# Performance work log

Measured on AMD Instinct MI355X. Metric: run time of the kernel, lower is better.

Reference implementation:

```python
import jax, jax.numpy as jnp
import numpy as np

N_NODES = 100000
N_EDGES = 1600000
D = 128
BN_EPS = 1e-5


def setup_inputs() -> dict:
    key = jax.random.key(0)
    ks = jax.random.split(key, 6)
    x = jax.random.normal(ks[0], (N_NODES, D), dtype=jnp.float32)
    edge_index = jax.random.randint(ks[1], (2, N_EDGES), 0, N_NODES, dtype=jnp.int64)
    s = 1.0 / np.sqrt(D)
    W1 = jax.random.uniform(ks[2], (D, D), jnp.float32, -s, s)
    W2 = jax.random.uniform(ks[3], (D, D), jnp.float32, -s, s)
    b1 = jnp.zeros((D,), jnp.float32)
    b2 = jnp.zeros((D,), jnp.float32)
    gamma = jnp.ones((D,), jnp.float32)
    beta = jnp.zeros((D,), jnp.float32)
    return {"x": x, "edge_index": edge_index, "W1": W1, "b1": b1,
            "W2": W2, "b2": b2, "gamma": gamma, "beta": beta}


def reference(x, edge_index, W1, b1, W2, b2, gamma, beta):
    src = edge_index[0]
    dst = edge_index[1]
    # GIN aggregation: (1+eps)*x + sum_{j in N(i)} x_j, eps = 0
    agg = jax.ops.segment_sum(x[src], dst, num_segments=x.shape[0])  # [N, D]
    h = agg + x
    # 2-layer MLP
    h = jax.nn.relu(h @ W1 + b1) @ W2 + b2
    # BatchNorm1d (training-mode batch stats, biased variance)
    mean = jnp.mean(h, axis=0)
    var = jnp.mean(jnp.square(h - mean), axis=0)
    h = (h - mean) * jax.lax.rsqrt(var + BN_EPS) * gamma + beta
    # residual; dropout p=0 -> identity
    return h + x
```

## Files before the change

### kernel.cpp

```cpp
#include <hip/hip_runtime.h>
#include <math.h>

#define NNODES 100000
#define NEDGES 1600000
#define DD 128
#define BN_EPS 1e-5f

#define NBUCK 98
#define BUCKW 1024
#define PBLK 512
#define PCHUNK 3125
#define NTILES 1563
#define FMM_GRID 512

typedef __attribute__((ext_vector_type(8))) short bf16x8;
typedef __attribute__((ext_vector_type(4))) float f32x4;
typedef __attribute__((ext_vector_type(2))) unsigned u32x2;
typedef __attribute__((ext_vector_type(4))) unsigned u32x4;

__device__ __forceinline__ unsigned short f2bf(float f) {
  unsigned u = __builtin_bit_cast(unsigned, f);
  u = (u + 0x7fffu + ((u >> 16) & 1u)) >> 16;
  return (unsigned short)u;
}
__device__ __forceinline__ float bfLO(unsigned u) {
  return __builtin_bit_cast(float, u << 16);
}
__device__ __forceinline__ float bfHI(unsigned u) {
  return __builtin_bit_cast(float, u & 0xffff0000u);
}


__global__ __launch_bounds__(256) void k_prep(const float* __restrict__ x,
                                              const float* __restrict__ W1,
                                              const float* __restrict__ W2,
                                              unsigned short* __restrict__ xb,
                                              unsigned short* __restrict__ wt1,
                                              unsigned short* __restrict__ wt2,
                                              float* __restrict__ bnAcc,
                                              const int* __restrict__ e32,
                                              int* __restrict__ cnt) {
  __shared__ int sc[NBUCK];
  int bid = blockIdx.x, tid = threadIdx.x;
  if (bid < 2) {
    const float* W = bid ? W2 : W1;
    unsigned short* wt = bid ? wt2 : wt1;
    if (tid < 128) {
      int n = tid;
      for (int k = 0; k < 128; ++k)
        wt[n * 128 + (k ^ ((n & 7) << 3))] = f2bf(W[k * 128 + n]);
    } else {
      bnAcc[(bid ? 0 : 128) + (tid - 128)] = 0.f;
    }
  } else if (bid < 6252) {
    long j = (long)(bid - 2) * 2048 + tid * 8;
    f32x4 a = __builtin_nontemporal_load((const f32x4*)(x + j));
    f32x4 b = __builtin_nontemporal_load((const f32x4*)(x + j + 4));
    u32x4 o;
    o.x = (unsigned)f2bf(a.x) | ((unsigned)f2bf(a.y) << 16);
    o.y = (unsigned)f2bf(a.z) | ((unsigned)f2bf(a.w) << 16);
    o.z = (unsigned)f2bf(b.x) | ((unsigned)f2bf(b.y) << 16);
    o.w = (unsigned)f2bf(b.z) | ((unsigned)f2bf(b.w) << 16);
    *(u32x4*)(xb + j) = o;
  } else {
    int blk = bid - 6252;
    int z = (tid < 64) ? (e32[2 * tid + 1] == 0) : 1;
    int is64 = __syncthreads_and(z);
    for (int i = tid; i < NBUCK; i += 256) sc[i] = 0;
    __syncthreads();
    const int* dstp = is64 ? (e32 + 2 * (long)NEDGES) : (e32 + NEDGES);
    long e0 = (long)blk * PCHUNK;
    for (int i = tid; i < PCHUNK; i += 256) {
      long e = e0 + i;
      int d = is64 ? dstp[2 * e] : dstp[e];
      atomicAdd(&sc[d >> 10], 1);
    }
    __syncthreads();
    for (int i = tid; i < NBUCK; i += 256) cnt[i * PBLK + blk] = sc[i];
  }
}

__global__ __launch_bounds__(256) void k_lscan(const int* __restrict__ cnt,
                                               int* __restrict__ off,
                                               int* __restrict__ bucketTot) {
  __shared__ int s[256];
  int b = blockIdx.x, tid = threadIdx.x;
  int v0 = cnt[b * PBLK + 2 * tid], v1 = cnt[b * PBLK + 2 * tid + 1];
  s[tid] = v0 + v1;
  __syncthreads();
  for (int o = 1; o < 256; o <<= 1) {
    int v = (tid >= o) ? s[tid - o] : 0;
    __syncthreads();
    s[tid] += v;
    __syncthreads();
  }
  int excl = s[tid] - v0 - v1;
  off[b * PBLK + 2 * tid] = excl;
  off[b * PBLK + 2 * tid + 1] = excl + v0;
  if (tid == 255) bucketTot[b] = s[255];
}

__global__ __launch_bounds__(256) void k_ppart(const int* __restrict__ e32,
                                               const int* __restrict__ off,
                                               const int* __restrict__ bucketTot,
                                               unsigned* __restrict__ stage) {
  __shared__ int cur[NBUCK];
  __shared__ int sbase[128];
  int tid = threadIdx.x, blk = blockIdx.x;
  int z = (tid < 64) ? (e32[2 * tid + 1] == 0) : 1;
  int is64 = __syncthreads_and(z);
  if (tid < 128) sbase[tid] = (tid < NBUCK) ? bucketTot[tid] : 0;
  __syncthreads();
  for (int o = 1; o < 128; o <<= 1) {
    int v = (tid >= o && tid < 128) ? sbase[tid - o] : 0;
    __syncthreads();
    if (tid < 128) sbase[tid] += v;
    __syncthreads();
  }
  if (tid < NBUCK)
    cur[tid] = off[tid * PBLK + blk] + ((tid == 0) ? 0 : sbase[tid - 1]);
  __syncthreads();
  const int* dstp = is64 ? (e32 + 2 * (long)NEDGES) : (e32 + NEDGES);
  long e0 = (long)blk * PCHUNK;
  for (int i = tid; i < PCHUNK; i += 256) {
    long e = e0 + i;
    int d = is64 ? dstp[2 * e] : dstp[e];
    int sv = is64 ? e32[2 * e] : e32[e];
    int pos = atomicAdd(&cur[d >> 10], 1);
    stage[pos] = ((unsigned)sv << 10) | (unsigned)(d & (BUCKW - 1));
  }
}

__global__ __launch_bounds__(256) void k_bucket(const unsigned* __restrict__ stage,
                                                const int* __restrict__ bucketTot,
                                                int* __restrict__ rowPtr,
                                                int* __restrict__ edgeSrc) {
  __shared__ int sdeg[BUCKW];
  __shared__ int srow[BUCKW];
  __shared__ int ss[256];
  __shared__ int sbase[128];
  int b = blockIdx.x, tid = threadIdx.x;
  if (tid < 128) sbase[tid] = (tid < NBUCK) ? bucketTot[tid] : 0;
  for (int i = tid; i < BUCKW; i += 256) sdeg[i] = 0;
  __syncthreads();
  for (int o = 1; o < 128; o <<= 1) {
    int v = (tid >= o && tid < 128) ? sbase[tid - o] : 0;
    __syncthreads();
    if (tid < 128) sbase[tid] += v;
    __syncthreads();
  }
  int base = (b == 0) ? 0 : sbase[b - 1];
  int tot = bucketTot[b];
  if (b == 0 && tid == 0) rowPtr[NNODES] = NEDGES;
  const unsigned* st = stage + base;
  for (int i = tid; i < tot; i += 256) atomicAdd(&sdeg[st[i] & (BUCKW - 1)], 1);
  __syncthreads();
  int j = tid * 4;
  int d0 = sdeg[j], d1 = sdeg[j + 1], d2 = sdeg[j + 2], d3 = sdeg[j + 3];
  int tsum = d0 + d1 + d2 + d3;
  ss[tid] = tsum;
  __syncthreads();
  for (int o = 1; o < 256; o <<= 1) {
    int v = (tid >= o) ? ss[tid - o] : 0;
    __syncthreads();
    ss[tid] += v;
    __syncthreads();
  }
  int excl = ss[tid] - tsum;
  srow[j] = excl;
  srow[j + 1] = excl + d0;
  srow[j + 2] = excl + d0 + d1;
  srow[j + 3] = excl + d0 + d1 + d2;
  __syncthreads();
  for (int i = tid; i < BUCKW; i += 256) {
    int dst = b * BUCKW + i;
    if (dst < NNODES) rowPtr[dst] = base + srow[i];
    sdeg[i] = srow[i];
  }
  __syncthreads();
  for (int i = tid; i < tot; i += 256) {
    unsigned p = st[i];
    int pos = atomicAdd(&sdeg[p & (BUCKW - 1)], 1);
    edgeSrc[base + pos] = (int)(p >> 10);
  }
}

__global__ __launch_bounds__(256) void k_gather(const u32x4* __restrict__ xb4,
                                                const int* __restrict__ rowPtr,
                                                const int* __restrict__ edgeSrc,
                                                u32x4* __restrict__ h0b4) {
  int node = (blockIdx.x * 256 + threadIdx.x) >> 6;
  int lane = threadIdx.x & 63;
  if (node >= NNODES) return;
  int li = lane & 15, q = lane >> 4;
  int beg = rowPtr[node], end = rowPtr[node + 1];
  float a0 = 0.f, a1 = 0.f, a2 = 0.f, a3 = 0.f;
  float a4 = 0.f, a5 = 0.f, a6 = 0.f, a7 = 0.f;
#define ACC8(v)                                              \
  a0 += bfLO((v).x); a1 += bfHI((v).x);                      \
  a2 += bfLO((v).y); a3 += bfHI((v).y);                      \
  a4 += bfLO((v).z); a5 += bfHI((v).z);                      \
  a6 += bfLO((v).w); a7 += bfHI((v).w);
  if (q == 0) {
    u32x4 u = xb4[(long)node * 16 + li];
    ACC8(u)
  }
  int e = beg;
  for (; e + 16 <= end; e += 16) {
    int s0 = edgeSrc[e + q];
    int s1 = edgeSrc[e + 4 + q];
    int s2 = edgeSrc[e + 8 + q];
    int s3 = edgeSrc[e + 12 + q];
    u32x4 v0 = xb4[(long)s0 * 16 + li];
    u32x4 v1 = xb4[(long)s1 * 16 + li];
    u32x4 v2 = xb4[(long)s2 * 16 + li];
    u32x4 v3 = xb4[(long)s3 * 16 + li];
    ACC8(v0) ACC8(v1) ACC8(v2) ACC8(v3)
  }
  if (e + 8 <= end) {
    int s0 = edgeSrc[e + q];
    int s1 = edgeSrc[e + 4 + q];
    u32x4 v0 = xb4[(long)s0 * 16 + li];
    u32x4 v1 = xb4[(long)s1 * 16 + li];
    ACC8(v0) ACC8(v1)
    e += 8;
  }
  for (; e < end; e += 4) {
    if (q < end - e) {
      int s = edgeSrc[e + q];
      u32x4 v = xb4[(long)s * 16 + li];
      ACC8(v)
    }
  }
#undef ACC8
  a0 += __shfl_xor(a0, 16, 64); a0 += __shfl_xor(a0, 32, 64);
  a1 += __shfl_xor(a1, 16, 64); a1 += __shfl_xor(a1, 32, 64);
  a2 += __shfl_xor(a2, 16, 64); a2 += __shfl_xor(a2, 32, 64);
  a3 += __shfl_xor(a3, 16, 64); a3 += __shfl_xor(a3, 32, 64);
  a4 += __shfl_xor(a4, 16, 64); a4 += __shfl_xor(a4, 32, 64);
  a5 += __shfl_xor(a5, 16, 64); a5 += __shfl_xor(a5, 32, 64);
  a6 += __shfl_xor(a6, 16, 64); a6 += __shfl_xor(a6, 32, 64);
  a7 += __shfl_xor(a7, 16, 64); a7 += __shfl_xor(a7, 32, 64);
  if (q == 0) {
    u32x4 o;
    o.x = (unsigned)f2bf(a0) | ((unsigned)f2bf(a1) << 16);
    o.y = (unsigned)f2bf(a2) | ((unsigned)f2bf(a3) << 16);
    o.z = (unsigned)f2bf(a4) | ((unsigned)f2bf(a5) << 16);
    o.w = (unsigned)f2bf(a6) | ((unsigned)f2bf(a7) << 16);
    h0b4[(long)node * 16 + li] = o;
  }
}

__global__ __launch_bounds__(256) void k_fmm(const unsigned short* Ab,
                                             const unsigned short* __restrict__ Wt1,
                                             const unsigned short* __restrict__ Wt2,
                                             const float* __restrict__ b1,
                                             const float* __restrict__ b2,
                                             unsigned short* Cb,
                                             float* __restrict__ bnSum,
                                             float* __restrict__ bnSq) {
  __shared__ __align__(16) char smem[81920];
  unsigned short* sW1 = (unsigned short*)smem;
  unsigned short* sW2 = (unsigned short*)(smem + 32768);
  unsigned short* sH  = (unsigned short*)(smem + 65536);
  float* sbn = (float*)(smem + 65536);
  int tid = threadIdx.x;
#pragma unroll
  for (int i = 0; i < 8; ++i) {
    ((u32x4*)sW1)[tid + 256 * i] = ((const u32x4*)Wt1)[tid + 256 * i];
    ((u32x4*)sW2)[tid + 256 * i] = ((const u32x4*)Wt2)[tid + 256 * i];
  }
  int w = tid >> 6, lane = tid & 63, l4 = lane >> 4, l15 = lane & 15;
  float bb1[8], bb2[8], ls[8], lq[8];
#pragma unroll
  for (int ni = 0; ni < 8; ++ni) {
    bb1[ni] = b1[ni * 16 + l15];
    bb2[ni] = b2[ni * 16 + l15];
    ls[ni] = 0.f; lq[ni] = 0.f;
  }

  int tile = blockIdx.x;
  bf16x8 af[4];
  {
    int r = tile * 64 + w * 16 + l15;
    if (r > NNODES - 1) r = NNODES - 1;
#pragma unroll
    for (int ks = 0; ks < 4; ++ks)
      af[ks] = __builtin_nontemporal_load(
          (const bf16x8*)(Ab + (long)r * 128 + ks * 32 + l4 * 8));
  }
  __syncthreads();

  while (tile < NTILES) {
    int next = tile + FMM_GRID;
    f32x4 acc[8];
#pragma unroll
    for (int ni = 0; ni < 8; ++ni) acc[ni] = (f32x4){0.f, 0.f, 0.f, 0.f};
#pragma unroll
    for (int ks = 0; ks < 4; ++ks)
#pragma unroll
      for (int ni = 0; ni < 8; ++ni) {
        int n = ni * 16 + l15, k = ks * 32 + l4 * 8;
        bf16x8 bf = *(const bf16x8*)(sW1 + n * 128 + (k ^ ((n & 7) << 3)));
        acc[ni] = __builtin_amdgcn_mfma_f32_16x16x32_bf16(af[ks], bf, acc[ni], 0, 0, 0);
      }
    __syncthreads();
#pragma unroll
    for (int ni = 0; ni < 8; ++ni) {
      int col = ni * 16 + l15;
#pragma unroll
      for (int rr = 0; rr < 4; ++rr) {
        int row = w * 16 + l4 * 4 + rr;
        float v = fmaxf(acc[ni][rr] + bb1[ni], 0.f);
        sH[row * 128 + (col ^ ((row & 7) << 3))] = f2bf(v);
      }
    }
    __syncthreads();
    bf16x8 afn[4] = {af[0], af[1], af[2], af[3]};
    if (next < NTILES) {
      int r = next * 64 + w * 16 + l15;
      if (r > NNODES - 1) r = NNODES - 1;
#pragma unroll
      for (int ks = 0; ks < 4; ++ks)
        afn[ks] = __builtin_nontemporal_load(
            (const bf16x8*)(Ab + (long)r * 128 + ks * 32 + l4 * 8));
    }
    bf16x8 a2[4];
    {
      int row = w * 16 + l15;
#pragma unroll
      for (int ks = 0; ks < 4; ++ks) {
        int k = ks * 32 + l4 * 8;
        a2[ks] = *(const bf16x8*)(sH + row * 128 + (k ^ ((row & 7) << 3)));
      }
    }
#pragma unroll
    for (int ni = 0; ni < 8; ++ni) acc[ni] = (f32x4){0.f, 0.f, 0.f, 0.f};
#pragma unroll
    for (int ks = 0; ks < 4; ++ks)
#pragma unroll
      for (int ni = 0; ni < 8; ++ni) {
        int n = ni * 16 + l15, k = ks * 32 + l4 * 8;
        bf16x8 bf = *(const bf16x8*)(sW2 + n * 128 + (k ^ ((n & 7) << 3)));
        acc[ni] = __builtin_amdgcn_mfma_f32_16x16x32_bf16(a2[ks], bf, acc[ni], 0, 0, 0);
      }
#pragma unroll
    for (int ni = 0; ni < 8; ++ni) {
      int n = ni * 16 + l15;
#pragma unroll
      for (int rr = 0; rr < 4; ++rr) {
        int row = tile * 64 + w * 16 + l4 * 4 + rr;
        if (row < NNODES) {
          float v = acc[ni][rr] + bb2[ni];
          __builtin_nontemporal_store(f2bf(v), Cb + (long)row * 128 + n);
          ls[ni] += v; lq[ni] += v * v;
        }
      }
    }
#pragma unroll
    for (int ks = 0; ks < 4; ++ks) af[ks] = afn[ks];
    tile = next;
  }

#pragma unroll
  for (int j = 0; j < 8; ++j) {
    ls[j] += __shfl_xor(ls[j], 16, 64); ls[j] += __shfl_xor(ls[j], 32, 64);
    lq[j] += __shfl_xor(lq[j], 16, 64); lq[j] += __shfl_xor(lq[j], 32, 64);
  }
  __syncthreads();
  if (l4 == 0) {
#pragma unroll
    for (int j = 0; j < 8; ++j) {
      sbn[w * 256 + j * 16 + l15] = ls[j];
      sbn[w * 256 + 128 + j * 16 + l15] = lq[j];
    }
  }
  __syncthreads();
  {
    float t = sbn[tid] + sbn[256 + tid] + sbn[512 + tid] + sbn[768 + tid];
    if (tid < 128) atomicAdd(&bnSum[tid], t);
    else atomicAdd(&bnSq[tid - 128], t);
  }
}

__global__ __launch_bounds__(256) void k_epi(const u32x4* __restrict__ h2b4,
                                             const u32x4* __restrict__ xb4,
                                             const float* __restrict__ bnSum,
                                             const float* __restrict__ bnSq,
                                             const float* __restrict__ gamma,
                                             const float* __restrict__ beta,
                                             f32x4* __restrict__ out4) {
  __shared__ float ssc[128], ssh[128];
  int tid = threadIdx.x;
  if (tid < 128) {
    float m = bnSum[tid] * (1.0f / NNODES);
    float var = bnSq[tid] * (1.0f / NNODES) - m * m;
    float sc = gamma[tid] * rsqrtf(var + BN_EPS);
    ssc[tid] = sc;
    ssh[tid] = beta[tid] - m * sc;
  }
  __syncthreads();
  long j = (long)blockIdx.x * 256 + tid;
  int c = (int)((j * 8) & 127);
  u32x4 h = __builtin_nontemporal_load(h2b4 + j);
  u32x4 xr = __builtin_nontemporal_load(xb4 + j);
  f32x4 sa = *(f32x4*)(ssc + c), sb = *(f32x4*)(ssc + c + 4);
  f32x4 fa = *(f32x4*)(ssh + c), fb = *(f32x4*)(ssh + c + 4);
  f32x4 oa, ob;
  oa.x = fmaf(bfLO(h.x), sa.x, fa.x) + bfLO(xr.x);
  oa.y = fmaf(bfHI(h.x), sa.y, fa.y) + bfHI(xr.x);
  oa.z = fmaf(bfLO(h.y), sa.z, fa.z) + bfLO(xr.y);
  oa.w = fmaf(bfHI(h.y), sa.w, fa.w) + bfHI(xr.y);
  ob.x = fmaf(bfLO(h.z), sb.x, fb.x) + bfLO(xr.z);
  ob.y = fmaf(bfHI(h.z), sb.y, fb.y) + bfHI(xr.z);
  ob.z = fmaf(bfLO(h.w), sb.z, fb.z) + bfLO(xr.w);
  ob.w = fmaf(bfHI(h.w), sb.w, fb.w) + bfHI(xr.w);
  __builtin_nontemporal_store(oa, out4 + 2 * j);
  __builtin_nontemporal_store(ob, out4 + 2 * j + 1);
}

extern "C" void kernel_launch(void* const* d_in, const int* in_sizes, int n_in,
                              void* d_out, int out_size, void* d_ws, size_t ws_size,
                              hipStream_t stream) {
  const float* x     = (const float*)d_in[0];
  const int*   e32   = (const int*)d_in[1];
  const float* W1    = (const float*)d_in[2];
  const float* b1    = (const float*)d_in[3];
  const float* W2    = (const float*)d_in[4];
  const float* b2    = (const float*)d_in[5];
  const float* gamma = (const float*)d_in[6];
  const float* beta  = (const float*)d_in[7];
  float* out = (float*)d_out;

  char* ws = (char*)d_ws;
  const size_t BFB = (size_t)NNODES * DD * 2;
  unsigned short* xb  = (unsigned short*)ws;
  unsigned short* h0b = (unsigned short*)(ws + BFB);
  unsigned short* h2b = h0b;

  int* rowPtr     = (int*)(ws + 3 * BFB);
  int* edgeSrc    = rowPtr + NNODES + 4;
  unsigned* stage = (unsigned*)(edgeSrc + NEDGES);
  int* cnt        = (int*)(stage + NEDGES);
  int* off        = cnt + NBUCK * PBLK;
  int* bucketTot  = off + NBUCK * PBLK;

  unsigned short* wt1 = (unsigned short*)(bucketTot + 256);
  unsigned short* wt2 = wt1 + 16384;
  float* bnSum = (float*)(wt2 + 16384);
  float* bnSq  = bnSum + 128;

  k_prep<<<6764, 256, 0, stream>>>(x, W1, W2, xb, wt1, wt2, bnSum, e32, cnt);
  k_lscan<<<NBUCK, 256, 0, stream>>>(cnt, off, bucketTot);
  k_ppart<<<PBLK, 256, 0, stream>>>(e32, off, bucketTot, stage);
  k_bucket<<<NBUCK, 256, 0, stream>>>(stage, bucketTot, rowPtr, edgeSrc);
  k_gather<<<25000, 256, 0, stream>>>((const u32x4*)xb, rowPtr, edgeSrc,
                                      (u32x4*)h0b);
  k_fmm<<<FMM_GRID, 256, 0, stream>>>(h0b, wt1, wt2, b1, b2, h2b, bnSum, bnSq);
  k_epi<<<6250, 256, 0, stream>>>((const u32x4*)h2b, (const u32x4*)xb, bnSum,
                                  bnSq, gamma, beta, (f32x4*)out);
}
```

Before: 196.0 us.

## Fuse BatchNorm epilogue into MLP kernel via grid-wide barrier

Merges the separate epilogue kernel into the fused-MLP kernel. After the BN statistics atomics, a software grid barrier (an atomic counter reset in the prep kernel) waits for all 512 blocks, then each block normalizes its own tiles and writes the output. The h2 bf16 stores become regular stores so they are likely to stay in cache for the epilogue re-read. This removes one kernel launch and may improve cache reuse of h2. In exchange it relies on all 512 blocks being co-resident, since the spin barrier deadlocks otherwise.

```diff
diff --git a/kernel.cpp b/kernel.cpp
--- a/kernel.cpp
+++ b/kernel.cpp
@@ -39,7 +39,8 @@
                                               unsigned short* __restrict__ wt2,
                                               float* __restrict__ bnAcc,
                                               const int* __restrict__ e32,
-                                              int* __restrict__ cnt) {
+                                              int* __restrict__ cnt,
+                                              int* __restrict__ bar) {
   __shared__ int sc[NBUCK];
   int bid = blockIdx.x, tid = threadIdx.x;
   if (bid < 2) {
@@ -51,6 +52,7 @@
         wt[n * 128 + (k ^ ((n & 7) << 3))] = f2bf(W[k * 128 + n]);
     } else {
       bnAcc[(bid ? 0 : 128) + (tid - 128)] = 0.f;
+      if (bid == 0 && tid == 128) *bar = 0;
     }
   } else if (bid < 6252) {
     long j = (long)(bid - 2) * 2048 + tid * 8;
@@ -252,13 +254,18 @@
 }
 
 __global__ __launch_bounds__(256) void k_fmm(const unsigned short* Ab,
+                                             const unsigned short* __restrict__ xb,
                                              const unsigned short* __restrict__ Wt1,
                                              const unsigned short* __restrict__ Wt2,
                                              const float* __restrict__ b1,
                                              const float* __restrict__ b2,
+                                             const float* __restrict__ gamma,
+                                             const float* __restrict__ beta,
                                              unsigned short* Cb,
                                              float* __restrict__ bnSum,
-                                             float* __restrict__ bnSq) {
+                                             float* __restrict__ bnSq,
+                                             int* __restrict__ bar,
+                                             float* __restrict__ outp) {
   __shared__ __align__(16) char smem[81920];
   unsigned short* sW1 = (unsigned short*)smem;
   unsigned short* sW2 = (unsigned short*)(smem + 32768);
@@ -352,7 +359,7 @@
         int row = tile * 64 + w * 16 + l4 * 4 + rr;
         if (row < NNODES) {
           float v = acc[ni][rr] + bb2[ni];
-          __builtin_nontemporal_store(f2bf(v), Cb + (long)row * 128 + n);
+          Cb[(long)row * 128 + n] = f2bf(v);
           ls[ni] += v; lq[ni] += v * v;
         }
       }
@@ -381,42 +388,58 @@
     if (tid < 128) atomicAdd(&bnSum[tid], t);
     else atomicAdd(&bnSq[tid - 128], t);
   }
-}
-
-__global__ __launch_bounds__(256) void k_epi(const u32x4* __restrict__ h2b4,
-                                             const u32x4* __restrict__ xb4,
-                                             const float* __restrict__ bnSum,
-                                             const float* __restrict__ bnSq,
-                                             const float* __restrict__ gamma,
-                                             const float* __restrict__ beta,
-                                             f32x4* __restrict__ out4) {
-  __shared__ float ssc[128], ssh[128];
-  int tid = threadIdx.x;
+
+  __threadfence();
+  __syncthreads();
+  if (tid == 0) {
+    __hip_atomic_fetch_add(bar, 1, __ATOMIC_ACQ_REL, __HIP_MEMORY_SCOPE_AGENT);
+    while (__hip_atomic_load(bar, __ATOMIC_ACQUIRE, __HIP_MEMORY_SCOPE_AGENT) <
+           FMM_GRID)
+      __builtin_amdgcn_s_sleep(8);
+  }
+  __syncthreads();
+
+  float* ssc = sbn;
+  float* ssh = sbn + 128;
   if (tid < 128) {
-    float m = bnSum[tid] * (1.0f / NNODES);
-    float var = bnSq[tid] * (1.0f / NNODES) - m * m;
+    float s = __hip_atomic_load(&bnSum[tid], __ATOMIC_RELAXED,
+                                __HIP_MEMORY_SCOPE_AGENT);
+    float sq = __hip_atomic_load(&bnSq[tid], __ATOMIC_RELAXED,
+                                 __HIP_MEMORY_SCOPE_AGENT);
+    float m = s * (1.0f / NNODES);
+    float var = sq * (1.0f / NNODES) - m * m;
     float sc = gamma[tid] * rsqrtf(var + BN_EPS);
     ssc[tid] = sc;
     ssh[tid] = beta[tid] - m * sc;
   }
   __syncthreads();
-  long j = (long)blockIdx.x * 256 + tid;
-  int c = (int)((j * 8) & 127);
-  u32x4 h = __builtin_nontemporal_load(h2b4 + j);
-  u32x4 xr = __builtin_nontemporal_load(xb4 + j);
-  f32x4 sa = *(f32x4*)(ssc + c), sb = *(f32x4*)(ssc + c + 4);
-  f32x4 fa = *(f32x4*)(ssh + c), fb = *(f32x4*)(ssh + c + 4);
-  f32x4 oa, ob;
-  oa.x = fmaf(bfLO(h.x), sa.x, fa.x) + bfLO(xr.x);
-  oa.y = fmaf(bfHI(h.x), sa.y, fa.y) + bfHI(xr.x);
-  oa.z = fmaf(bfLO(h.y), sa.z, fa.z) + bfLO(xr.y);
-  oa.w = fmaf(bfHI(h.y), sa.w, fa.w) + bfHI(xr.y);
-  ob.x = fmaf(bfLO(h.z), sb.x, fb.x) + bfLO(xr.z);
-  ob.y = fmaf(bfHI(h.z), sb.y, fb.y) + bfHI(xr.z);
-  ob.z = fmaf(bfLO(h.w), sb.z, fb.z) + bfLO(xr.w);
-  ob.w = fmaf(bfHI(h.w), sb.w, fb.w) + bfHI(xr.w);
-  __builtin_nontemporal_store(oa, out4 + 2 * j);
-  __builtin_nontemporal_store(ob, out4 + 2 * j + 1);
+
+  int r = tid >> 2, u = tid & 3;
+  for (int t = blockIdx.x; t < NTILES; t += FMM_GRID) {
+    int row = t * 64 + r;
+    if (row < NNODES) {
+#pragma unroll
+      for (int p = 0; p < 4; ++p) {
+        int c = u * 32 + p * 8;
+        u32x4 h = *(const u32x4*)(Cb + (long)row * 128 + c);
+        u32x4 xr = *(const u32x4*)(xb + (long)row * 128 + c);
+        f32x4 sa = *(f32x4*)(ssc + c), sb = *(f32x4*)(ssc + c + 4);
+        f32x4 fa = *(f32x4*)(ssh + c), fb = *(f32x4*)(ssh + c + 4);
+        f32x4 oa, ob;
+        oa.x = fmaf(bfLO(h.x), sa.x, fa.x) + bfLO(xr.x);
+        oa.y = fmaf(bfHI(h.x), sa.y, fa.y) + bfHI(xr.x);
+        oa.z = fmaf(bfLO(h.y), sa.z, fa.z) + bfLO(xr.y);
+        oa.w = fmaf(bfHI(h.y), sa.w, fa.w) + bfHI(xr.y);
+        ob.x = fmaf(bfLO(h.z), sb.x, fb.x) + bfLO(xr.z);
+        ob.y = fmaf(bfHI(h.z), sb.y, fb.y) + bfHI(xr.z);
+        ob.z = fmaf(bfLO(h.w), sb.z, fb.z) + bfLO(xr.w);
+        ob.w = fmaf(bfHI(h.w), sb.w, fb.w) + bfHI(xr.w);
+        __builtin_nontemporal_store(oa, (f32x4*)(outp + (long)row * 128 + c));
+        __builtin_nontemporal_store(ob,
+                                    (f32x4*)(outp + (long)row * 128 + c + 4));
+      }
+    }
+  }
 }
 
 extern "C" void kernel_launch(void* const* d_in, const int* in_sizes, int n_in,
@@ -449,14 +472,15 @@
   unsigned short* wt2 = wt1 + 16384;
   float* bnSum = (float*)(wt2 + 16384);
   float* bnSq  = bnSum + 128;
-
-  k_prep<<<6764, 256, 0, stream>>>(x, W1, W2, xb, wt1, wt2, bnSum, e32, cnt);
+  int*   bar   = (int*)(bnSq + 128);
+
+  k_prep<<<6764, 256, 0, stream>>>(x, W1, W2, xb, wt1, wt2, bnSum, e32, cnt,
+                                   bar);
   k_lscan<<<NBUCK, 256, 0, stream>>>(cnt, off, bucketTot);
   k_ppart<<<PBLK, 256, 0, stream>>>(e32, off, bucketTot, stage);
   k_bucket<<<NBUCK, 256, 0, stream>>>(stage, bucketTot, rowPtr, edgeSrc);
   k_gather<<<25000, 256, 0, stream>>>((const u32x4*)xb, rowPtr, edgeSrc,
                                       (u32x4*)h0b);
-  k_fmm<<<FMM_GRID, 256, 0, stream>>>(h0b, wt1, wt2, b1, b2, h2b, bnSum, bnSq);
-  k_epi<<<6250, 256, 0, stream>>>((const u32x4*)h2b, (const u32x4*)xb, bnSum,
-                                  bnSq, gamma, beta, (f32x4*)out);
-}
+  k_fmm<<<FMM_GRID, 256, 0, stream>>>(h0b, xb, wt1, wt2, b1, b2, gamma, beta,
+                                      h2b, bnSum, bnSq, bar, out);
+}
```

New measurement: 349.5 us. 78.3% more time.
